# Performance work log

Hardware: AMD Instinct MI355X
Metric: run time of the kernel (lower is better)

The kernel has to match this reference:

```python
import jax, jax.numpy as jnp
import numpy as np

B, S, E, H, Dh = 1, 2048, 1024, 16, 64


def setup_inputs() -> dict:
    key = jax.random.key(0)
    ks = jax.random.split(key, 9)
    sc = 0.02
    return {
        "x": jax.random.normal(ks[0], (B, S, E), jnp.float32),
        "Wq": jax.random.normal(ks[1], (H, E, Dh), jnp.float32) * sc,
        "bq": jax.random.normal(ks[2], (H, Dh), jnp.float32) * sc,
        "Wk": jax.random.normal(ks[3], (H, E, Dh), jnp.float32) * sc,
        "bk": jax.random.normal(ks[4], (H, Dh), jnp.float32) * sc,
        "Wv": jax.random.normal(ks[5], (H, E, Dh), jnp.float32) * sc,
        "bv": jax.random.normal(ks[6], (H, Dh), jnp.float32) * sc,
        "Wo": jax.random.normal(ks[7], (E, E), jnp.float32) * sc,
        "bo": jax.random.normal(ks[8], (E,), jnp.float32) * sc,
    }


def reference(x, Wq, bq, Wk, bk, Wv, bv, Wo, bo):
    # Per-head projections (stacked): [B,S,E] x [H,E,Dh] -> [B,H,S,Dh]
    q = jnp.einsum("bse,hed->bhsd", x, Wq) + bq[None, :, None, :]
    k = jnp.einsum("bse,hed->bhsd", x, Wk) + bk[None, :, None, :]
    v = jnp.einsum("bse,hed->bhsd", x, Wv) + bv[None, :, None, :]
    scores = jnp.einsum("bhsd,bhtd->bhst", q, k) / np.sqrt(Dh).astype(np.float32)
    causal = jnp.tril(jnp.ones((S, S), dtype=bool))  # [S,S]
    scores = jnp.where(causal[None, None], scores, -jnp.inf)
    attn = jax.nn.softmax(scores, axis=-1)  # attn_dropout p=0 -> identity
    out = jnp.einsum("bhst,bhtd->bhsd", attn, v)
    # concat heads in head order: [B,S,H*Dh]
    out = out.transpose(0, 2, 1, 3).reshape(B, S, H * Dh)
    return out @ Wo.T if False else jnp.einsum("bsf,ef->bse", out, Wo.T.T * 0 + Wo) if False else out @ Wo.swapaxes(0, 1) * 0 + (jnp.einsum("bsf,fe->bse", out, Wo) + bo)
```

## Files before the change

kernel.cpp:

```cpp
#include <hip/hip_runtime.h>
#include <hip/hip_bf16.h>

#define S_LEN 2048
#define E_DIM 1024
#define NH 16
#define DH 64

typedef __bf16 v8bf __attribute__((ext_vector_type(8)));
typedef __bf16 v4bf __attribute__((ext_vector_type(4)));
typedef float f32x4 __attribute__((ext_vector_type(4)));
typedef unsigned short u16x4 __attribute__((ext_vector_type(4)));
typedef unsigned short u16x8 __attribute__((ext_vector_type(8)));

__device__ __align__(16) unsigned short g_Xb[S_LEN * E_DIM];
__device__ __align__(16) unsigned short g_WT[3 * E_DIM * E_DIM];
__device__ __align__(16) unsigned short g_WoT[E_DIM * E_DIM];
__device__ __align__(16) unsigned short g_Qb[NH * S_LEN * DH];
__device__ __align__(16) unsigned short g_Kb[NH * S_LEN * DH];
__device__ __align__(16) unsigned short g_Vt[NH * DH * S_LEN];
__device__ __align__(16) unsigned short g_AO[S_LEN * E_DIM];

__device__ inline unsigned short f2bf(float f) {
    unsigned int u = __float_as_uint(f);
    u += 0x7FFF + ((u >> 16) & 1);
    return (unsigned short)(u >> 16);
}
__device__ inline f32x4 mfma16(v8bf a, v8bf b, f32x4 c) {
    return __builtin_amdgcn_mfma_f32_16x16x32_bf16(a, b, c, 0, 0, 0);
}
__device__ inline f32x4 mfma16k16(v4bf a, v4bf b, f32x4 c) {
#if __has_builtin(__builtin_amdgcn_mfma_f32_16x16x16_bf16)
    return __builtin_amdgcn_mfma_f32_16x16x16_bf16(a, b, c, 0, 0, 0);
#elif __has_builtin(__builtin_amdgcn_mfma_f32_16x16x16bf16_1k)
    typedef short s4v __attribute__((ext_vector_type(4)));
    union UA { v4bf v; s4v s; };
    UA ua, ub; ua.v = a; ub.v = b;
    return __builtin_amdgcn_mfma_f32_16x16x16bf16_1k(ua.s, ub.s, c, 0, 0, 0);
#else
    asm("v_mfma_f32_16x16x16_bf16 %0, %1, %2, %0" : "+v"(c) : "v"(a), "v"(b));
    return c;
#endif
}

typedef __attribute__((address_space(3))) unsigned int lds_u32;
typedef __attribute__((address_space(1))) const unsigned int glb_u32;
__device__ inline void async_cp16(const unsigned short* g, unsigned short* l) {
    __builtin_amdgcn_global_load_lds((glb_u32*)g, (lds_u32*)l, 16, 0, 0);
}

__global__ __launch_bounds__(256) void prep(const float* __restrict__ X,
                                            const float* __restrict__ Wq,
                                            const float* __restrict__ Wk,
                                            const float* __restrict__ Wv,
                                            const float* __restrict__ Wo) {
    __shared__ __align__(16) unsigned short lds[64 * 72];
    const int b = blockIdx.x;
    const int t = threadIdx.x;
    if (b < 2048) {
        int i = b * 256 + t;
        f32x4 v = reinterpret_cast<const f32x4*>(X)[i];
        u16x4 o = {f2bf(v.x), f2bf(v.y), f2bf(v.z), f2bf(v.w)};
        reinterpret_cast<u16x4*>(g_Xb)[i] = o;
    } else if (b < 2304) {
        int bb = b - 2048;
        const int h = bb >> 4;
        const int e0 = (bb & 15) * 64;
        const float* srcs[3] = {Wq, Wk, Wv};
#pragma unroll
        for (int tn = 0; tn < 3; tn++) {
            const float* W = srcs[tn] + h * 65536;
#pragma unroll
            for (int p = 0; p < 4; p++) {
                int e = p * 16 + (t >> 4);
                int d = (t & 15) * 4;
                f32x4 v = *reinterpret_cast<const f32x4*>(&W[(e0 + e) * 64 + d]);
                lds[(d + 0) * 72 + e] = f2bf(v.x);
                lds[(d + 1) * 72 + e] = f2bf(v.y);
                lds[(d + 2) * 72 + e] = f2bf(v.z);
                lds[(d + 3) * 72 + e] = f2bf(v.w);
            }
            __syncthreads();
#pragma unroll
            for (int p = 0; p < 2; p++) {
                int d = p * 32 + (t >> 3);
                int ec = (t & 7) * 8;
                u16x8 o = *reinterpret_cast<const u16x8*>(&lds[d * 72 + ec]);
                *reinterpret_cast<u16x8*>(&g_WT[(tn * 1024 + h * 64 + d) * E_DIM + e0 + ec]) = o;
            }
            __syncthreads();
        }
    } else {
        int bb = b - 2304;
        const int f0 = (bb >> 4) * 64;
        const int e0 = (bb & 15) * 64;
#pragma unroll
        for (int p = 0; p < 4; p++) {
            int f = p * 16 + (t >> 4);
            int e = (t & 15) * 4;
            f32x4 v = *reinterpret_cast<const f32x4*>(&Wo[(f0 + f) * E_DIM + e0 + e]);
            lds[(e + 0) * 72 + f] = f2bf(v.x);
            lds[(e + 1) * 72 + f] = f2bf(v.y);
            lds[(e + 2) * 72 + f] = f2bf(v.z);
            lds[(e + 3) * 72 + f] = f2bf(v.w);
        }
        __syncthreads();
#pragma unroll
        for (int p = 0; p < 2; p++) {
            int e = p * 32 + (t >> 3);
            int fc = (t & 7) * 8;
            u16x8 o = *reinterpret_cast<const u16x8*>(&lds[e * 72 + fc]);
            *reinterpret_cast<u16x8*>(&g_WoT[(e0 + e) * E_DIM + f0 + fc]) = o;
        }
    }
}

__global__ __launch_bounds__(256) void qkv_gemm(const float* __restrict__ bq,
                                                const float* __restrict__ bk,
                                                const float* __restrict__ bv) {
    __shared__ __align__(16) unsigned short lds[24576];
    const int t = threadIdx.x;
    const int wave = t >> 6;
    const int lane = t & 63;
    const int m = lane & 15, quad = lane >> 4;
    const int s0 = blockIdx.x * 128;
    const int n0 = blockIdx.y * 64;

    const int rl = t >> 3;
    const int cx = (t & 7) ^ (rl & 7);
    const int axor = m & 7;

    f32x4 acc[2][4];
#pragma unroll
    for (int i = 0; i < 2; i++)
#pragma unroll
        for (int j = 0; j < 4; j++) acc[i][j] = (f32x4){0.f, 0.f, 0.f, 0.f};

    const unsigned short* gA = g_Xb + (s0 + rl) * E_DIM + cx * 8;
    const unsigned short* gB = g_WT + (n0 + rl) * E_DIM + cx * 8;

    auto stage = [&](int k0, int buf) {
        unsigned short* lA = lds + buf * 12288;
        unsigned short* lB = lA + 8192;
        const unsigned short* ga = gA + k0;
        async_cp16(ga,              lA + wave * 512);
        async_cp16(ga + 32 * E_DIM, lA + 2048 + wave * 512);
        async_cp16(ga + 64 * E_DIM, lA + 4096 + wave * 512);
        async_cp16(ga + 96 * E_DIM, lA + 6144 + wave * 512);
        const unsigned short* gb = gB + k0;
        async_cp16(gb,              lB + wave * 512);
        async_cp16(gb + 32 * E_DIM, lB + 2048 + wave * 512);
    };

    stage(0, 0);
    __syncthreads();
    int buf = 0;
    for (int k0 = 0; k0 < E_DIM; k0 += 64) {
        if (k0 + 64 < E_DIM) stage(k0 + 64, buf ^ 1);
        const unsigned short* lA = lds + buf * 12288;
        const unsigned short* lB = lA + 8192;
        const unsigned short* lAr0 = lA + (wave * 32 + m) * 64;
        const unsigned short* lAr1 = lAr0 + 16 * 64;
#pragma unroll
        for (int ks = 0; ks < 2; ks++) {
            const int ch = ((ks * 4 + quad) ^ axor) * 8;
            v8bf a0 = *reinterpret_cast<const v8bf*>(lAr0 + ch);
            v8bf a1 = *reinterpret_cast<const v8bf*>(lAr1 + ch);
#pragma unroll
            for (int j = 0; j < 4; j++) {
                v8bf bfr = *reinterpret_cast<const v8bf*>(lB + (j * 16 + m) * 64 + ch);
                acc[0][j] = mfma16(a0, bfr, acc[0][j]);
                acc[1][j] = mfma16(a1, bfr, acc[1][j]);
            }
        }
        __syncthreads();
        buf ^= 1;
    }

    const int tensor = n0 >> 10;
    const int nn0 = n0 & 1023;
    const int hh = nn0 >> 6;
    const float* bb = tensor == 0 ? bq : (tensor == 1 ? bk : bv);
    float bias[4];
#pragma unroll
    for (int j = 0; j < 4; j++) bias[j] = bb[nn0 + j * 16 + m];

    if (tensor < 2) {
#pragma unroll
        for (int i = 0; i < 2; i++)
#pragma unroll
            for (int j = 0; j < 4; j++)
#pragma unroll
                for (int r = 0; r < 4; r++) {
                    int sl = wave * 32 + i * 16 + quad * 4 + r;
                    int nl = j * 16 + m;
                    lds[sl * 72 + nl] = f2bf(acc[i][j][r] + bias[j]);
                }
        __syncthreads();
        if (tensor == 0) {
            unsigned short* dst = g_Qb + (hh * S_LEN + s0) * DH;
#pragma unroll
            for (int p = 0; p < 4; p++) {
                int row = p * 32 + (t >> 3);
                int c = t & 7;
                u16x8 v = *reinterpret_cast<const u16x8*>(&lds[row * 72 + c * 8]);
                *reinterpret_cast<u16x8*>(&dst[row * DH + c * 8]) = v;
            }
        } else {
            unsigned short* dst = g_Kb + hh * S_LEN * DH;
            const int tb0 = s0 >> 4;
#pragma unroll
            for (int p = 0; p < 4; p++) {
                int row = p * 32 + (t >> 3);
                int c = t & 7;
                u16x8 v = *reinterpret_cast<const u16x8*>(&lds[row * 72 + c * 8]);
                int idx = (tb0 + (row >> 4)) * 1024 + (c >> 2) * 512 + (row & 15) * 32 + (c & 3) * 8;
                *reinterpret_cast<u16x8*>(&dst[idx]) = v;
            }
        }
    } else {
#pragma unroll
        for (int i = 0; i < 2; i++)
#pragma unroll
            for (int j = 0; j < 4; j++)
#pragma unroll
                for (int r = 0; r < 4; r++) {
                    int sl = wave * 32 + i * 16 + quad * 4 + r;
                    int nl = j * 16 + m;
                    lds[nl * 136 + sl] = f2bf(acc[i][j][r] + bias[j]);
                }
        __syncthreads();
        unsigned short* dst = g_Vt + hh * S_LEN * DH;
#pragma unroll
        for (int p = 0; p < 4; p++) {
            int nl = p * 16 + (t >> 4);
            int sc = t & 15;
            u16x8 v = *reinterpret_cast<const u16x8*>(&lds[nl * 136 + sc * 8]);
            int idx = ((s0 >> 4) + (sc >> 1)) * 1024 + (nl >> 4) * 256 + (nl & 15) * 16 + (sc & 1) * 8;
            *reinterpret_cast<u16x8*>(&dst[idx]) = v;
        }
    }
}

__global__ __launch_bounds__(256) void flash_attn() {
    __shared__ __align__(16) float comb[256 * 20];
    const int t = threadIdx.x;
    const int wave = t >> 6, lane = t & 63;
    const int m = lane & 15, quad = lane >> 4;
    const int h = blockIdx.x & 15;
    const int Tp = blockIdx.x >> 4;
    const int qq = Tp >> 4, tt = Tp & 15;
    const int T = (qq == 0) ? tt : (qq == 1) ? 31 - tt : (qq == 2) ? 32 + tt : 63 - tt;
    const int s0 = T * 32;

    const unsigned short* Qh = g_Qb + h * S_LEN * DH;
    const unsigned short* Kh = g_Kb + h * S_LEN * DH;
    const unsigned short* Vh = g_Vt + h * S_LEN * DH;
    const int ko = m * 32 + quad * 8;
    const int vo = m * 16 + quad * 4;
    const int tq = quad * 4;

    v8bf aqA0 = *reinterpret_cast<const v8bf*>(Qh + (s0 + m) * DH + quad * 8);
    v8bf aqA1 = *reinterpret_cast<const v8bf*>(Qh + (s0 + m) * DH + 32 + quad * 8);
    v8bf aqB0 = *reinterpret_cast<const v8bf*>(Qh + (s0 + 16 + m) * DH + quad * 8);
    v8bf aqB1 = *reinterpret_cast<const v8bf*>(Qh + (s0 + 16 + m) * DH + 32 + quad * 8);

    f32x4 oA[4], oB[4];
#pragma unroll
    for (int i = 0; i < 4; i++) { oA[i] = (f32x4){0.f,0.f,0.f,0.f}; oB[i] = (f32x4){0.f,0.f,0.f,0.f}; }
    float lA = 0.f, lB = 0.f;

    const float SC = 0.125f * 1.44269504088896f;
    const int tEnd = s0 + 32;

    int t0 = wave * 64;
    v8bf kf[4][2];
    v4bf vf[4][4];
    if (t0 < tEnd) {
        const unsigned short* kb = Kh + t0 * 64 + ko;
#pragma unroll
        for (int ct = 0; ct < 4; ct++) {
            kf[ct][0] = *reinterpret_cast<const v8bf*>(kb + ct * 1024);
            kf[ct][1] = *reinterpret_cast<const v8bf*>(kb + ct * 1024 + 512);
        }
        const unsigned short* vb = Vh + t0 * 64 + vo;
#pragma unroll
        for (int dt = 0; dt < 4; dt++)
#pragma unroll
            for (int ct = 0; ct < 4; ct++)
                vf[dt][ct] = *reinterpret_cast<const v4bf*>(vb + ct * 1024 + dt * 256);
    }

    for (; t0 < tEnd; t0 += 256) {
        const bool doA = (t0 < s0 + 16);
        const int t1 = t0 + 256;

        __builtin_amdgcn_s_setprio(1);
        f32x4 sB[4];
#pragma unroll
        for (int ct = 0; ct < 4; ct++) {
            sB[ct] = (f32x4){0.f,0.f,0.f,0.f};
            sB[ct] = mfma16(kf[ct][0], aqB0, sB[ct]);
            sB[ct] = mfma16(kf[ct][1], aqB1, sB[ct]);
        }
        __builtin_amdgcn_s_setprio(0);
        v4bf ptB[4];
#pragma unroll
        for (int ct = 0; ct < 4; ct++) {
            const int tb = t0 + ct * 16 + tq;
            if (t0 + ct * 16 + 15 > s0 + 16) {
#pragma unroll
                for (int r = 0; r < 4; r++)
                    if (tb + r > s0 + 16 + m) sB[ct][r] = -3e38f;
            }
#pragma unroll
            for (int r = 0; r < 4; r++)
                sB[ct][r] = __builtin_amdgcn_exp2f(sB[ct][r] * SC);
            lB += sB[ct][0] + sB[ct][1] + sB[ct][2] + sB[ct][3];
            __hip_bfloat162 b01 = __float22bfloat162_rn(make_float2(sB[ct][0], sB[ct][1]));
            __hip_bfloat162 b23 = __float22bfloat162_rn(make_float2(sB[ct][2], sB[ct][3]));
            union { unsigned int u[2]; v4bf v; } pk;
            pk.u[0] = *reinterpret_cast<unsigned int*>(&b01);
            pk.u[1] = *reinterpret_cast<unsigned int*>(&b23);
            ptB[ct] = pk.v;
        }
        __builtin_amdgcn_s_setprio(1);
#pragma unroll
        for (int dt = 0; dt < 4; dt++)
#pragma unroll
            for (int ct = 0; ct < 4; ct++)
                oB[dt] = mfma16k16(vf[dt][ct], ptB[ct], oB[dt]);
        __builtin_amdgcn_s_setprio(0);

        f32x4 sA[4];
        if (doA) {
            __builtin_amdgcn_s_setprio(1);
#pragma unroll
            for (int ct = 0; ct < 4; ct++) {
                sA[ct] = (f32x4){0.f,0.f,0.f,0.f};
                sA[ct] = mfma16(kf[ct][0], aqA0, sA[ct]);
                sA[ct] = mfma16(kf[ct][1], aqA1, sA[ct]);
            }
            __builtin_amdgcn_s_setprio(0);
        }
        if (t1 < tEnd) {
            const unsigned short* kb = Kh + t1 * 64 + ko;
#pragma unroll
            for (int ct = 0; ct < 4; ct++) {
                kf[ct][0] = *reinterpret_cast<const v8bf*>(kb + ct * 1024);
                kf[ct][1] = *reinterpret_cast<const v8bf*>(kb + ct * 1024 + 512);
            }
        }

        if (doA) {
            v4bf ptA[4];
#pragma unroll
            for (int ct = 0; ct < 4; ct++) {
                const int tb = t0 + ct * 16 + tq;
                if (t0 + ct * 16 + 15 > s0) {
#pragma unroll
                    for (int r = 0; r < 4; r++)
                        if (tb + r > s0 + m) sA[ct][r] = -3e38f;
                }
#pragma unroll
                for (int r = 0; r < 4; r++)
                    sA[ct][r] = __builtin_amdgcn_exp2f(sA[ct][r] * SC);
                lA += sA[ct][0] + sA[ct][1] + sA[ct][2] + sA[ct][3];
                __hip_bfloat162 b01 = __float22bfloat162_rn(make_float2(sA[ct][0], sA[ct][1]));
                __hip_bfloat162 b23 = __float22bfloat162_rn(make_float2(sA[ct][2], sA[ct][3]));
                union { unsigned int u[2]; v4bf v; } pk;
                pk.u[0] = *reinterpret_cast<unsigned int*>(&b01);
                pk.u[1] = *reinterpret_cast<unsigned int*>(&b23);
                ptA[ct] = pk.v;
            }
            __builtin_amdgcn_s_setprio(1);
#pragma unroll
            for (int dt = 0; dt < 4; dt++)
#pragma unroll
                for (int ct = 0; ct < 4; ct++)
                    oA[dt] = mfma16k16(vf[dt][ct], ptA[ct], oA[dt]);
            __builtin_amdgcn_s_setprio(0);
        }

        if (t1 < tEnd) {
            const unsigned short* vb = Vh + t1 * 64 + vo;
#pragma unroll
            for (int dt = 0; dt < 4; dt++)
#pragma unroll
                for (int ct = 0; ct < 4; ct++)
                    vf[dt][ct] = *reinterpret_cast<const v4bf*>(vb + ct * 1024 + dt * 256);
        }
    }

    float* cw = comb + t * 20;
#pragma unroll
    for (int dt = 0; dt < 4; dt++) *reinterpret_cast<f32x4*>(cw + dt * 4) = oA[dt];
    cw[16] = lA;
    __syncthreads();
    {
        f32x4 os = (f32x4){0.f,0.f,0.f,0.f};
        float ls = 0.f;
#pragma unroll
        for (int w = 0; w < 4; w++) {
            const float* cr = comb + (w * 64 + lane) * 20;
            os += *reinterpret_cast<const f32x4*>(cr + wave * 4);
#pragma unroll
            for (int q2 = 0; q2 < 4; q2++)
                ls += comb[(w * 64 + q2 * 16 + m) * 20 + 16];
        }
        float inv = 1.0f / ls;
        u16x4 ov = {f2bf(os[0] * inv), f2bf(os[1] * inv), f2bf(os[2] * inv), f2bf(os[3] * inv)};
        *reinterpret_cast<u16x4*>(&g_AO[(s0 + m) * E_DIM + h * 64 + wave * 16 + quad * 4]) = ov;
    }
    __syncthreads();
#pragma unroll
    for (int dt = 0; dt < 4; dt++) *reinterpret_cast<f32x4*>(cw + dt * 4) = oB[dt];
    cw[16] = lB;
    __syncthreads();
    {
        f32x4 os = (f32x4){0.f,0.f,0.f,0.f};
        float ls = 0.f;
#pragma unroll
        for (int w = 0; w < 4; w++) {
            const float* cr = comb + (w * 64 + lane) * 20;
            os += *reinterpret_cast<const f32x4*>(cr + wave * 4);
#pragma unroll
            for (int q2 = 0; q2 < 4; q2++)
                ls += comb[(w * 64 + q2 * 16 + m) * 20 + 16];
        }
        float inv = 1.0f / ls;
        u16x4 ov = {f2bf(os[0] * inv), f2bf(os[1] * inv), f2bf(os[2] * inv), f2bf(os[3] * inv)};
        *reinterpret_cast<u16x4*>(&g_AO[(s0 + 16 + m) * E_DIM + h * 64 + wave * 16 + quad * 4]) = ov;
    }
}

__global__ __launch_bounds__(256) void out_gemm(const float* __restrict__ bo,
                                                float* __restrict__ OUT) {
    __shared__ __align__(16) unsigned short lds[24576];
    const int t = threadIdx.x;
    const int wave = t >> 6;
    const int lane = t & 63;
    const int m = lane & 15, quad = lane >> 4;
    const int s0 = blockIdx.x * 128;
    const int n0 = blockIdx.y * 64;

    const int rl = t >> 3;
    const int cx = (t & 7) ^ (rl & 7);
    const int axor = m & 7;

    f32x4 acc[2][4];
#pragma unroll
    for (int i = 0; i < 2; i++)
#pragma unroll
        for (int j = 0; j < 4; j++) acc[i][j] = (f32x4){0.f, 0.f, 0.f, 0.f};

    const unsigned short* gA = g_AO + (s0 + rl) * E_DIM + cx * 8;
    const unsigned short* gB = g_WoT + (n0 + rl) * E_DIM + cx * 8;

    auto stage = [&](int k0, int buf) {
        unsigned short* lA = lds + buf * 12288;
        unsigned short* lB = lA + 8192;
        const unsigned short* ga = gA + k0;
        async_cp16(ga,              lA + wave * 512);
        async_cp16(ga + 32 * E_DIM, lA + 2048 + wave * 512);
        async_cp16(ga + 64 * E_DIM, lA + 4096 + wave * 512);
        async_cp16(ga + 96 * E_DIM, lA + 6144 + wave * 512);
        const unsigned short* gb = gB + k0;
        async_cp16(gb,              lB + wave * 512);
        async_cp16(gb + 32 * E_DIM, lB + 2048 + wave * 512);
    };

    stage(0, 0);
    __syncthreads();
    int buf = 0;
    for (int k0 = 0; k0 < E_DIM; k0 += 64) {
        if (k0 + 64 < E_DIM) stage(k0 + 64, buf ^ 1);
        const unsigned short* lA = lds + buf * 12288;
        const unsigned short* lB = lA + 8192;
        const unsigned short* lAr0 = lA + (wave * 32 + m) * 64;
        const unsigned short* lAr1 = lAr0 + 16 * 64;
#pragma unroll
        for (int ks = 0; ks < 2; ks++) {
            const int ch = ((ks * 4 + quad) ^ axor) * 8;
            v8bf a0 = *reinterpret_cast<const v8bf*>(lAr0 + ch);
            v8bf a1 = *reinterpret_cast<const v8bf*>(lAr1 + ch);
#pragma unroll
            for (int j = 0; j < 4; j++) {
                v8bf bfr = *reinterpret_cast<const v8bf*>(lB + (j * 16 + m) * 64 + ch);
                acc[0][j] = mfma16(a0, bfr, acc[0][j]);
                acc[1][j] = mfma16(a1, bfr, acc[1][j]);
            }
        }
        __syncthreads();
        buf ^= 1;
    }
#pragma unroll
    for (int i = 0; i < 2; i++)
#pragma unroll
        for (int j = 0; j < 4; j++) {
            int e = n0 + j * 16 + m;
            float bias = bo[e];
#pragma unroll
            for (int r = 0; r < 4; r++) {
                int s = s0 + wave * 32 + i * 16 + quad * 4 + r;
                OUT[s * E_DIM + e] = acc[i][j][r] + bias;
            }
        }
}

extern "C" void kernel_launch(void* const* d_in, const int* in_sizes, int n_in,
                              void* d_out, int out_size, void* d_ws, size_t ws_size,
                              hipStream_t stream) {
    (void)in_sizes; (void)n_in; (void)out_size; (void)d_ws; (void)ws_size;
    const float* x  = (const float*)d_in[0];
    const float* Wq = (const float*)d_in[1];
    const float* bq = (const float*)d_in[2];
    const float* Wk = (const float*)d_in[3];
    const float* bk = (const float*)d_in[4];
    const float* Wv = (const float*)d_in[5];
    const float* bv = (const float*)d_in[6];
    const float* Wo = (const float*)d_in[7];
    const float* bo = (const float*)d_in[8];
    float* out = (float*)d_out;

    hipLaunchKernelGGL(prep,       dim3(2560),   dim3(256), 0, stream, x, Wq, Wk, Wv, Wo);
    hipLaunchKernelGGL(qkv_gemm,   dim3(16, 48), dim3(256), 0, stream, bq, bk, bv);
    hipLaunchKernelGGL(flash_attn, dim3(1024),   dim3(256), 0, stream);
    hipLaunchKernelGGL(out_gemm,   dim3(16, 16), dim3(256), 0, stream, bo, out);
}
```

Baseline: 156.1 us.

## Process 64 query rows per attention block to reuse K/V fragments

Each flash-attention block now handles four 16-row query subtiles (64 rows) instead of two, so every K and V fragment loaded from global memory is reused across four query tiles, halving K/V traffic per query row. The grid is halved to 512 blocks, and the block order is remapped to pair short and long causal ranges for load balance. The cost is more accumulator registers (16 f32x4 outputs plus 8 Q fragments), which may reduce occupancy, and fewer blocks to spread across CUs.

Measured after the change: 159.9 us. +2.5%, slower.

```diff
diff --git a/kernel.cpp b/kernel.cpp
--- a/kernel.cpp
+++ b/kernel.cpp
@@ -248,9 +248,8 @@
     const int m = lane & 15, quad = lane >> 4;
     const int h = blockIdx.x & 15;
     const int Tp = blockIdx.x >> 4;
-    const int qq = Tp >> 4, tt = Tp & 15;
-    const int T = (qq == 0) ? tt : (qq == 1) ? 31 - tt : (qq == 2) ? 32 + tt : 63 - tt;
-    const int s0 = T * 32;
+    const int B = (Tp < 16) ? Tp : 47 - Tp;
+    const int s0 = B * 64;
 
     const unsigned short* Qh = g_Qb + h * S_LEN * DH;
     const unsigned short* Kh = g_Kb + h * S_LEN * DH;
@@ -259,18 +258,23 @@
     const int vo = m * 16 + quad * 4;
     const int tq = quad * 4;
 
-    v8bf aqA0 = *reinterpret_cast<const v8bf*>(Qh + (s0 + m) * DH + quad * 8);
-    v8bf aqA1 = *reinterpret_cast<const v8bf*>(Qh + (s0 + m) * DH + 32 + quad * 8);
-    v8bf aqB0 = *reinterpret_cast<const v8bf*>(Qh + (s0 + 16 + m) * DH + quad * 8);
-    v8bf aqB1 = *reinterpret_cast<const v8bf*>(Qh + (s0 + 16 + m) * DH + 32 + quad * 8);
-
-    f32x4 oA[4], oB[4];
-#pragma unroll
-    for (int i = 0; i < 4; i++) { oA[i] = (f32x4){0.f,0.f,0.f,0.f}; oB[i] = (f32x4){0.f,0.f,0.f,0.f}; }
-    float lA = 0.f, lB = 0.f;
+    v8bf aq[4][2];
+#pragma unroll
+    for (int sub = 0; sub < 4; sub++) {
+        const unsigned short* qp = Qh + (s0 + sub * 16 + m) * DH + quad * 8;
+        aq[sub][0] = *reinterpret_cast<const v8bf*>(qp);
+        aq[sub][1] = *reinterpret_cast<const v8bf*>(qp + 32);
+    }
+
+    f32x4 o[4][4];
+#pragma unroll
+    for (int sub = 0; sub < 4; sub++)
+#pragma unroll
+        for (int dt = 0; dt < 4; dt++) o[sub][dt] = (f32x4){0.f,0.f,0.f,0.f};
+    float l[4] = {0.f, 0.f, 0.f, 0.f};
 
     const float SC = 0.125f * 1.44269504088896f;
-    const int tEnd = s0 + 32;
+    const int tEnd = s0 + 64;
 
     int t0 = wave * 64;
     v8bf kf[4][2];
@@ -291,96 +295,57 @@
     }
 
     for (; t0 < tEnd; t0 += 256) {
-        const bool doA = (t0 < s0 + 16);
         const int t1 = t0 + 256;
-
-        __builtin_amdgcn_s_setprio(1);
-        f32x4 sB[4];
-#pragma unroll
-        for (int ct = 0; ct < 4; ct++) {
-            sB[ct] = (f32x4){0.f,0.f,0.f,0.f};
-            sB[ct] = mfma16(kf[ct][0], aqB0, sB[ct]);
-            sB[ct] = mfma16(kf[ct][1], aqB1, sB[ct]);
-        }
-        __builtin_amdgcn_s_setprio(0);
-        v4bf ptB[4];
-#pragma unroll
-        for (int ct = 0; ct < 4; ct++) {
-            const int tb = t0 + ct * 16 + tq;
-            if (t0 + ct * 16 + 15 > s0 + 16) {
-#pragma unroll
-                for (int r = 0; r < 4; r++)
-                    if (tb + r > s0 + 16 + m) sB[ct][r] = -3e38f;
-            }
-#pragma unroll
-            for (int r = 0; r < 4; r++)
-                sB[ct][r] = __builtin_amdgcn_exp2f(sB[ct][r] * SC);
-            lB += sB[ct][0] + sB[ct][1] + sB[ct][2] + sB[ct][3];
-            __hip_bfloat162 b01 = __float22bfloat162_rn(make_float2(sB[ct][0], sB[ct][1]));
-            __hip_bfloat162 b23 = __float22bfloat162_rn(make_float2(sB[ct][2], sB[ct][3]));
-            union { unsigned int u[2]; v4bf v; } pk;
-            pk.u[0] = *reinterpret_cast<unsigned int*>(&b01);
-            pk.u[1] = *reinterpret_cast<unsigned int*>(&b23);
-            ptB[ct] = pk.v;
-        }
-        __builtin_amdgcn_s_setprio(1);
-#pragma unroll
-        for (int dt = 0; dt < 4; dt++)
-#pragma unroll
-            for (int ct = 0; ct < 4; ct++)
-                oB[dt] = mfma16k16(vf[dt][ct], ptB[ct], oB[dt]);
-        __builtin_amdgcn_s_setprio(0);
-
-        f32x4 sA[4];
-        if (doA) {
-            __builtin_amdgcn_s_setprio(1);
-#pragma unroll
-            for (int ct = 0; ct < 4; ct++) {
-                sA[ct] = (f32x4){0.f,0.f,0.f,0.f};
-                sA[ct] = mfma16(kf[ct][0], aqA0, sA[ct]);
-                sA[ct] = mfma16(kf[ct][1], aqA1, sA[ct]);
-            }
-            __builtin_amdgcn_s_setprio(0);
-        }
-        if (t1 < tEnd) {
-            const unsigned short* kb = Kh + t1 * 64 + ko;
-#pragma unroll
-            for (int ct = 0; ct < 4; ct++) {
-                kf[ct][0] = *reinterpret_cast<const v8bf*>(kb + ct * 1024);
-                kf[ct][1] = *reinterpret_cast<const v8bf*>(kb + ct * 1024 + 512);
-            }
-        }
-
-        if (doA) {
-            v4bf ptA[4];
-#pragma unroll
-            for (int ct = 0; ct < 4; ct++) {
-                const int tb = t0 + ct * 16 + tq;
-                if (t0 + ct * 16 + 15 > s0) {
+#pragma unroll
+        for (int sub = 0; sub < 4; sub++) {
+            const int qb = s0 + sub * 16;
+            if (t0 <= qb + 15) {
+                __builtin_amdgcn_s_setprio(1);
+                f32x4 s[4];
+#pragma unroll
+                for (int ct = 0; ct < 4; ct++) {
+                    s[ct] = (f32x4){0.f,0.f,0.f,0.f};
+                    s[ct] = mfma16(kf[ct][0], aq[sub][0], s[ct]);
+                    s[ct] = mfma16(kf[ct][1], aq[sub][1], s[ct]);
+                }
+                __builtin_amdgcn_s_setprio(0);
+                if (sub == 3 && t1 < tEnd) {
+                    const unsigned short* kb = Kh + t1 * 64 + ko;
+#pragma unroll
+                    for (int ct = 0; ct < 4; ct++) {
+                        kf[ct][0] = *reinterpret_cast<const v8bf*>(kb + ct * 1024);
+                        kf[ct][1] = *reinterpret_cast<const v8bf*>(kb + ct * 1024 + 512);
+                    }
+                }
+                v4bf pt[4];
+#pragma unroll
+                for (int ct = 0; ct < 4; ct++) {
+                    const int tb = t0 + ct * 16 + tq;
+                    if (t0 + ct * 16 + 15 > qb) {
+#pragma unroll
+                        for (int r = 0; r < 4; r++)
+                            if (tb + r > qb + m) s[ct][r] = -3e38f;
+                    }
 #pragma unroll
                     for (int r = 0; r < 4; r++)
-                        if (tb + r > s0 + m) sA[ct][r] = -3e38f;
+                        s[ct][r] = __builtin_amdgcn_exp2f(s[ct][r] * SC);
+                    l[sub] += s[ct][0] + s[ct][1] + s[ct][2] + s[ct][3];
+                    __hip_bfloat162 b01 = __float22bfloat162_rn(make_float2(s[ct][0], s[ct][1]));
+                    __hip_bfloat162 b23 = __float22bfloat162_rn(make_float2(s[ct][2], s[ct][3]));
+                    union { unsigned int u[2]; v4bf v; } pk;
+                    pk.u[0] = *reinterpret_cast<unsigned int*>(&b01);
+                    pk.u[1] = *reinterpret_cast<unsigned int*>(&b23);
+                    pt[ct] = pk.v;
                 }
-#pragma unroll
-                for (int r = 0; r < 4; r++)
-                    sA[ct][r] = __builtin_amdgcn_exp2f(sA[ct][r] * SC);
-                lA += sA[ct][0] + sA[ct][1] + sA[ct][2] + sA[ct][3];
-                __hip_bfloat162 b01 = __float22bfloat162_rn(make_float2(sA[ct][0], sA[ct][1]));
-                __hip_bfloat162 b23 = __float22bfloat162_rn(make_float2(sA[ct][2], sA[ct][3]));
-                union { unsigned int u[2]; v4bf v; } pk;
-                pk.u[0] = *reinterpret_cast<unsigned int*>(&b01);
-                pk.u[1] = *reinterpret_cast<unsigned int*>(&b23);
-                ptA[ct] = pk.v;
-            }
-            __builtin_amdgcn_s_setprio(1);
-#pragma unroll
-            for (int dt = 0; dt < 4; dt++)
-#pragma unroll
-                for (int ct = 0; ct < 4; ct++)
-                    oA[dt] = mfma16k16(vf[dt][ct], ptA[ct], oA[dt]);
-            __builtin_amdgcn_s_setprio(0);
-        }
-
+                __builtin_amdgcn_s_setprio(1);
+#pragma unroll
+                for (int dt = 0; dt < 4; dt++)
+#pragma unroll
+                    for (int ct = 0; ct < 4; ct++)
+                        o[sub][dt] = mfma16k16(vf[dt][ct], pt[ct], o[sub][dt]);
+                __builtin_amdgcn_s_setprio(0);
+            }
+        }
         if (t1 < tEnd) {
             const unsigned short* vb = Vh + t1 * 64 + vo;
 #pragma unroll
@@ -393,10 +358,12 @@
 
     float* cw = comb + t * 20;
 #pragma unroll
-    for (int dt = 0; dt < 4; dt++) *reinterpret_cast<f32x4*>(cw + dt * 4) = oA[dt];
-    cw[16] = lA;
-    __syncthreads();
-    {
+    for (int sub = 0; sub < 4; sub++) {
+        if (sub) __syncthreads();
+#pragma unroll
+        for (int dt = 0; dt < 4; dt++) *reinterpret_cast<f32x4*>(cw + dt * 4) = o[sub][dt];
+        cw[16] = l[sub];
+        __syncthreads();
         f32x4 os = (f32x4){0.f,0.f,0.f,0.f};
         float ls = 0.f;
 #pragma unroll
@@ -409,27 +376,7 @@
         }
         float inv = 1.0f / ls;
         u16x4 ov = {f2bf(os[0] * inv), f2bf(os[1] * inv), f2bf(os[2] * inv), f2bf(os[3] * inv)};
-        *reinterpret_cast<u16x4*>(&g_AO[(s0 + m) * E_DIM + h * 64 + wave * 16 + quad * 4]) = ov;
-    }
-    __syncthreads();
-#pragma unroll
-    for (int dt = 0; dt < 4; dt++) *reinterpret_cast<f32x4*>(cw + dt * 4) = oB[dt];
-    cw[16] = lB;
-    __syncthreads();
-    {
-        f32x4 os = (f32x4){0.f,0.f,0.f,0.f};
-        float ls = 0.f;
-#pragma unroll
-        for (int w = 0; w < 4; w++) {
-            const float* cr = comb + (w * 64 + lane) * 20;
-            os += *reinterpret_cast<const f32x4*>(cr + wave * 4);
-#pragma unroll
-            for (int q2 = 0; q2 < 4; q2++)
-                ls += comb[(w * 64 + q2 * 16 + m) * 20 + 16];
-        }
-        float inv = 1.0f / ls;
-        u16x4 ov = {f2bf(os[0] * inv), f2bf(os[1] * inv), f2bf(os[2] * inv), f2bf(os[3] * inv)};
-        *reinterpret_cast<u16x4*>(&g_AO[(s0 + 16 + m) * E_DIM + h * 64 + wave * 16 + quad * 4]) = ov;
+        *reinterpret_cast<u16x4*>(&g_AO[(s0 + sub * 16 + m) * E_DIM + h * 64 + wave * 16 + quad * 4]) = ov;
     }
 }
 
@@ -524,6 +471,6 @@
 
     hipLaunchKernelGGL(prep,       dim3(2560),   dim3(256), 0, stream, x, Wq, Wk, Wv, Wo);
     hipLaunchKernelGGL(qkv_gemm,   dim3(16, 48), dim3(256), 0, stream, bq, bk, bv);
-    hipLaunchKernelGGL(flash_attn, dim3(1024),   dim3(256), 0, stream);
+    hipLaunchKernelGGL(flash_attn, dim3(512),    dim3(256), 0, stream);
     hipLaunchKernelGGL(out_gemm,   dim3(16, 16), dim3(256), 0, stream, bo, out);
 }
```
